# Kernel optimization log

Measured on AMD Instinct MI355X. Metric: run time of the kernel, lower is better.

The kernel has to match this reference:

```python
import jax, jax.numpy as jnp
import numpy as np

HID = 1024
H = 8        # num_attention_heads
KV = 2       # num_key_value_heads
HD = HID // H  # head_dim = 128
G = H // KV    # kv groups = 4
EPS = 1e-6


def setup_inputs() -> dict:
    key = jax.random.key(0)
    ks = jax.random.split(key, 12)
    B, S = 4, 2048
    s = 0.02
    inp = {
        "hidden_states": jax.random.normal(ks[0], (B, S, HID), jnp.float32),
        "rope": jax.random.normal(ks[1], (1, 1, S, 2 * HD), jnp.float32),
        # q_proj outputs 2*H*HD (query + elementwise gate)
        "Wq": jax.random.normal(ks[2], (HID, 2 * H * HD), jnp.float32) * s,
        "bq": jnp.zeros((2 * H * HD,), jnp.float32),
        "Wk": jax.random.normal(ks[3], (HID, KV * HD), jnp.float32) * s,
        "bk": jnp.zeros((KV * HD,), jnp.float32),
        "Wv": jax.random.normal(ks[4], (HID, KV * HD), jnp.float32) * s,
        "bv": jnp.zeros((KV * HD,), jnp.float32),
        "Wo": jax.random.normal(ks[5], (H * HD, HID), jnp.float32) * s,
        "bo": jnp.zeros((HID,), jnp.float32),
        "q_norm_w": jnp.ones((HD,), jnp.float32),
        "k_norm_w": jnp.ones((HD,), jnp.float32),
    }
    return inp


def _rmsnorm(x, w):
    var = jnp.mean(jnp.square(x), axis=-1, keepdims=True)
    return x * jax.lax.rsqrt(var + EPS) * w


def _rot(x):
    # interleaved rotation: [-x1, x0, -x3, x2, ...]
    x2 = x.reshape(x.shape[:-1] + (HD // 2, 2))
    r = jnp.stack([-x2[..., 1], x2[..., 0]], axis=-1)
    return r.reshape(x.shape)


def _apply_rope_cat(x, emb):
    # emb: [S, 2*HD] = cat(sin, cos); x: [B, h, S, HD]
    sin, cos = jnp.split(emb, 2, axis=-1)
    sin = sin[None, None]
    cos = cos[None, None]
    return x * cos + _rot(x) * sin


def reference(hidden_states, rope, Wq, bq, Wk, bk, Wv, bv, Wo, bo, q_norm_w, k_norm_w):
    B, S, _ = hidden_states.shape
    qg = hidden_states @ Wq + bq                     # [B,S,2*H*HD]
    qg = qg.reshape(B, S, KV, -1)                    # [B,S,KV, 2*G*HD]
    q, gate = jnp.split(qg, [HD * G], axis=-1)       # [B,S,KV,G*HD], [B,S,KV,G*HD]
    gate = gate.reshape(B, S, H, HD)                 # [B,S,H,HD]
    q = q.reshape(B, S, H, HD).transpose(0, 2, 1, 3) # [B,H,S,HD]
    k = (hidden_states @ Wk + bk).reshape(B, S, KV, HD).transpose(0, 2, 1, 3)
    v = (hidden_states @ Wv + bv).reshape(B, S, KV, HD).transpose(0, 2, 1, 3)

    q = _rmsnorm(q, q_norm_w)
    k = _rmsnorm(k, k_norm_w)

    emb = rope[0, 0, :S]                             # [S, 2*HD]
    q = _apply_rope_cat(q, emb)
    k = _apply_rope_cat(k, emb)

    # GQA: repeat kv heads to match query heads
    k = jnp.repeat(k, G, axis=1)                     # [B,H,S,HD]
    v = jnp.repeat(v, G, axis=1)

    scale = 1.0 / jnp.sqrt(jnp.asarray(HD, q.dtype))
    scores = jnp.einsum("bhqd,bhkd->bhqk", q, k) * scale
    attn = jax.nn.softmax(scores, axis=-1)
    out = jnp.einsum("bhqk,bhkd->bhqd", attn, v)     # [B,H,S,HD]

    out = out.transpose(0, 2, 1, 3)                  # [B,S,H,HD]
    out = out * jax.nn.sigmoid(gate)
    out = out.reshape(B, S, H * HD)
    return out @ Wo + bo
```

## Files before the change

### kernel.cpp

```cpp
#include <hip/hip_runtime.h>
#include <math.h>

#define SCALE_ 0.08838834764831845f
#define PSHIFT 8.0f

typedef __attribute__((ext_vector_type(8))) short short8;
typedef __attribute__((ext_vector_type(4))) float floatx4;
typedef __attribute__((ext_vector_type(4))) _Float16 half4;
typedef __attribute__((ext_vector_type(8))) _Float16 half8;

__device__ inline short f2bf(float x) {
    union { float f; unsigned u; } v; v.f = x;
    unsigned r = v.u + 0x7fff + ((v.u >> 16) & 1);
    return (short)(r >> 16);
}
__device__ inline float bf2f(short h) {
    union { float f; unsigned u; } v; v.u = ((unsigned)(unsigned short)h) << 16;
    return v.f;
}

__global__ __launch_bounds__(256) void prep_fused(
    const float* __restrict__ X, short* __restrict__ Xb,
    const float* __restrict__ bq, const float* __restrict__ bk2,
    const float* __restrict__ bv2, float* __restrict__ bcat,
    const float* __restrict__ Wq, const float* __restrict__ Wk,
    const float* __restrict__ Wv, const float* __restrict__ Wo,
    short* __restrict__ Wt, short* __restrict__ Wot)
{
    __shared__ float T[32][33];
    const int bid = blockIdx.x;
    const int t = threadIdx.x;
    if (bid < 8192) {
        const int gid = bid * 256 + t;
        if (gid < 2097152) {
            const float4 v = ((const float4*)X)[gid];
            short4 o;
            o.x = f2bf(v.x); o.y = f2bf(v.y); o.z = f2bf(v.z); o.w = f2bf(v.w);
            ((short4*)Xb)[gid] = o;
        }
        if (gid < 2560)
            bcat[gid] = (gid < 2048) ? bq[gid]
                      : (gid < 2304) ? bk2[gid - 2048] : bv2[gid - 2304];
        return;
    }
    const int t2 = bid - 8192;
    const int k0 = (t2 & 31) * 32;
    const int ny = t2 >> 5;
    const float* src; int ldn, ncol0, nrow0; short* dst;
    if (ny < 80) {
        const int n0 = ny * 32;
        if (n0 < 2048)      { src = Wq; ldn = 2048; ncol0 = n0; }
        else if (n0 < 2304) { src = Wk; ldn = 256;  ncol0 = n0 - 2048; }
        else                { src = Wv; ldn = 256;  ncol0 = n0 - 2304; }
        dst = Wt; nrow0 = n0;
    } else {
        const int n0 = (ny - 80) * 32;
        src = Wo; ldn = 1024; ncol0 = n0; dst = Wot; nrow0 = n0;
    }
    {
        const int r = t >> 3, c4 = (t & 7) * 4;
        const float4 v = *(const float4*)&src[(size_t)(k0 + r) * ldn + ncol0 + c4];
        T[r][c4 + 0] = v.x; T[r][c4 + 1] = v.y; T[r][c4 + 2] = v.z; T[r][c4 + 3] = v.w;
    }
    __syncthreads();
    {
        const int nr = t >> 3, kc4 = (t & 7) * 4;
        short4 o;
        o.x = f2bf(T[kc4 + 0][nr]);
        o.y = f2bf(T[kc4 + 1][nr]);
        o.z = f2bf(T[kc4 + 2][nr]);
        o.w = f2bf(T[kc4 + 3][nr]);
        *(short4*)&dst[(size_t)(nrow0 + nr) * 1024 + k0 + kc4] = o;
    }
}

__global__ __launch_bounds__(256) void qkv_mfma(
    const short* __restrict__ Ag, const short* __restrict__ Bg,
    const float* __restrict__ bcat,
    short* __restrict__ qb, short* __restrict__ kb,
    short* __restrict__ vb, short* __restrict__ gateb)
{
    __shared__ short As[128 * 64];
    __shared__ short Bs[128 * 64];
    const int tid = threadIdx.x;
    const int wave = tid >> 6, lane = tid & 63;
    const int quad = lane >> 4, l16 = lane & 15;
    const int wm = wave & 1, wn = wave >> 1;
    const int lin = blockIdx.x;
    const int xcd = lin & 7;
    const int idx = lin >> 3;
    const int rr_ = idx / 20;
    const int m0 = (xcd * 8 + rr_) * 128;
    const int n0 = (idx - rr_ * 20) * 128;

    floatx4 acc[4][4] = {};

    for (int k0 = 0; k0 < 1024; k0 += 64) {
        __syncthreads();
        #pragma unroll
        for (int c = 0; c < 4; ++c) {
            const int blk = (c * 4 + wave) * 64 + lane;
            const int row = blk >> 3, p = blk & 7;
            const int col = (p ^ (row & 7)) << 3;
            __builtin_amdgcn_global_load_lds(
                (const __attribute__((address_space(1))) unsigned int*)(Ag + (size_t)(m0 + row) * 1024 + k0 + col),
                (__attribute__((address_space(3))) unsigned int*)&As[(c * 4 + wave) * 512],
                16, 0, 0);
            __builtin_amdgcn_global_load_lds(
                (const __attribute__((address_space(1))) unsigned int*)(Bg + (size_t)(n0 + row) * 1024 + k0 + col),
                (__attribute__((address_space(3))) unsigned int*)&Bs[(c * 4 + wave) * 512],
                16, 0, 0);
        }
        __syncthreads();
        #pragma unroll
        for (int ks = 0; ks < 2; ++ks) {
            short8 af[4], bfr[4];
            #pragma unroll
            for (int mt = 0; mt < 4; ++mt) {
                const int row = wm * 64 + mt * 16 + l16;
                const int p = (ks * 4 + quad) ^ (row & 7);
                af[mt] = *(const short8*)&As[row * 64 + p * 8];
            }
            #pragma unroll
            for (int nt = 0; nt < 4; ++nt) {
                const int row = wn * 64 + nt * 16 + l16;
                const int p = (ks * 4 + quad) ^ (row & 7);
                bfr[nt] = *(const short8*)&Bs[row * 64 + p * 8];
            }
            #pragma unroll
            for (int mt = 0; mt < 4; ++mt)
                #pragma unroll
                for (int nt = 0; nt < 4; ++nt)
                    acc[mt][nt] = __builtin_amdgcn_mfma_f32_16x16x32_bf16(af[mt], bfr[nt], acc[mt][nt], 0, 0, 0);
        }
    }

    #pragma unroll
    for (int nt = 0; nt < 4; ++nt) {
        const int n = n0 + wn * 64 + nt * 16 + l16;
        const float bias = bcat[n];
        #pragma unroll
        for (int mt = 0; mt < 4; ++mt) {
            #pragma unroll
            for (int r = 0; r < 4; ++r) {
                const int m = m0 + wm * 64 + mt * 16 + quad * 4 + r;
                const int b = m >> 11, s = m & 2047;
                const short o = f2bf(acc[mt][nt][r] + bias);
                if (n < 2048) {
                    const int kv = n >> 10, rr = n & 1023;
                    if (rr < 512) {
                        const int h = kv * 4 + (rr >> 7), d = rr & 127;
                        qb[(((size_t)(b * 8 + h)) * 2048 + s) * 128 + d] = o;
                    } else {
                        const int r2 = rr - 512;
                        const int h = kv * 4 + (r2 >> 7), d = r2 & 127;
                        gateb[(size_t)m * 1024 + h * 128 + d] = o;
                    }
                } else if (n < 2304) {
                    const int c = n - 2048;
                    kb[(((size_t)(b * 2 + (c >> 7))) * 2048 + s) * 128 + (c & 127)] = o;
                } else {
                    const int c = n - 2304;
                    vb[(((size_t)(b * 2 + (c >> 7))) * 2048 + s) * 128 + (c & 127)] = o;
                }
            }
        }
    }
}

__global__ __launch_bounds__(256) void norm_vtrans(
    short* __restrict__ qb, short* __restrict__ kb,
    const float* __restrict__ rope,
    const float* __restrict__ qw, const float* __restrict__ kw,
    const short* __restrict__ vb, _Float16* __restrict__ vt)
{
    __shared__ float T[32][33];
    const int bid = blockIdx.x;
    const int t = threadIdx.x;
    if (bid < 20480) {
        const int row = bid * 4 + (t >> 6);
        short* base; const float* w; int s; float scl;
        if (row < 65536) { base = qb + (size_t)row * 128; s = row & 2047; w = qw; scl = SCALE_; }
        else { const int r2 = row - 65536; base = kb + (size_t)r2 * 128; s = r2 & 2047; w = kw; scl = 1.0f; }
        const int lane = t & 63;
        const short2 xv = *(const short2*)&base[lane * 2];
        const float x0 = bf2f(xv.x), x1 = bf2f(xv.y);
        float ssq = x0 * x0 + x1 * x1;
        #pragma unroll
        for (int off = 1; off < 64; off <<= 1) ssq += __shfl_xor(ssq, off);
        const float inv = rsqrtf(ssq * (1.0f / 128.0f) + 1e-6f);
        const float a = x0 * inv * w[lane * 2];
        const float b = x1 * inv * w[lane * 2 + 1];
        const float* er = rope + (size_t)s * 256;
        const float sin0 = er[lane * 2], sin1 = er[lane * 2 + 1];
        const float cos0 = er[128 + lane * 2], cos1 = er[128 + lane * 2 + 1];
        short2 o;
        o.x = f2bf((a * cos0 - b * sin0) * scl);
        o.y = f2bf((b * cos1 + a * sin1) * scl);
        *(short2*)&base[lane * 2] = o;
        return;
    }
    const int t2 = bid - 20480;
    const int s0 = (t2 & 63) * 32, d0 = ((t2 >> 6) & 3) * 32, bk = t2 >> 8;
    const short* src = vb + ((size_t)bk * 2048 + s0) * 128 + d0;
    {
        const int sr = t >> 3, c4 = (t & 7) * 4;
        const short4 xv = *(const short4*)&src[sr * 128 + c4];
        T[sr][c4 + 0] = bf2f(xv.x);
        T[sr][c4 + 1] = bf2f(xv.y);
        T[sr][c4 + 2] = bf2f(xv.z);
        T[sr][c4 + 3] = bf2f(xv.w);
    }
    __syncthreads();
    {
        const int dr = t >> 3, sc4 = (t & 7) * 4;
        const int cs = sc4 >> 2;
        const int nc = (cs < 4) ? (cs << 1) : (((cs - 4) << 1) | 1);
        half4 o;
        o[0] = (_Float16)T[sc4 + 0][dr];
        o[1] = (_Float16)T[sc4 + 1][dr];
        o[2] = (_Float16)T[sc4 + 2][dr];
        o[3] = (_Float16)T[sc4 + 3][dr];
        *(half4*)&vt[((size_t)bk * 128 + d0 + dr) * 2048 + s0 + nc * 4] = o;
    }
}

__global__ __launch_bounds__(256, 2) void attn_mfma(
    const short* __restrict__ qb, const short* __restrict__ kb,
    const _Float16* __restrict__ vt, const short* __restrict__ gateb,
    short* __restrict__ xo)
{
    __shared__ short    Ks[2][64 * 128];
    __shared__ _Float16 VTs[2][128 * 64];

    const int tid = threadIdx.x;
    const int wave = tid >> 6, lane = tid & 63;
    const int quad = lane >> 4, l16 = lane & 15;
    const int bh = blockIdx.y, b = bh >> 3, h = bh & 7, kv = h >> 2;
    const int q0 = blockIdx.x * 128;

    short8 qf[4][2];
    #pragma unroll
    for (int u = 0; u < 2; ++u) {
        const short* qbase = qb + (((size_t)(b * 8 + h)) * 2048 + q0 + wave * 32 + u * 16 + l16) * 128;
        #pragma unroll
        for (int ks = 0; ks < 4; ++ks)
            qf[ks][u] = *(const short8*)&qbase[ks * 32 + quad * 8];
    }

    const short*    kbase  = kb + (size_t)(b * 2 + kv) * 2048 * 128;
    const _Float16* vtbase = vt + (size_t)(b * 2 + kv) * 128 * 2048;

    int koff[4], voff[4];
    #pragma unroll
    for (int c = 0; c < 4; ++c) {
        const int sidx = (c * 4 + wave) * 64 + lane;
        { const int r = sidx >> 4, p = sidx & 15;
          koff[c] = r * 128 + ((p ^ (r & 7)) << 3); }
        { const int r = sidx >> 3, p = sidx & 7;
          voff[c] = r * 2048 + ((p ^ (r & 7)) << 3); }
    }

    floatx4 O[8][2] = {};
    float lsum[2] = {0.0f, 0.0f};

    #pragma unroll
    for (int c = 0; c < 4; ++c) {
        __builtin_amdgcn_global_load_lds(
            (const __attribute__((address_space(1))) unsigned int*)(kbase + koff[c]),
            (__attribute__((address_space(3))) unsigned int*)&Ks[0][(c * 4 + wave) * 512],
            16, 0, 0);
        __builtin_amdgcn_global_load_lds(
            (const __attribute__((address_space(1))) unsigned int*)(vtbase + voff[c]),
            (__attribute__((address_space(3))) unsigned int*)&VTs[0][(c * 4 + wave) * 512],
            16, 0, 0);
    }

    for (int kt = 0; kt < 32; ++kt) {
        const int cur = kt & 1;
        __syncthreads();

        if (kt + 1 < 32) {
            const short*    kg = kbase  + (size_t)(kt + 1) * 8192;
            const _Float16* vg = vtbase + (kt + 1) * 64;
            #pragma unroll
            for (int c = 0; c < 4; ++c) {
                __builtin_amdgcn_global_load_lds(
                    (const __attribute__((address_space(1))) unsigned int*)(kg + koff[c]),
                    (__attribute__((address_space(3))) unsigned int*)&Ks[cur ^ 1][(c * 4 + wave) * 512],
                    16, 0, 0);
                __builtin_amdgcn_global_load_lds(
                    (const __attribute__((address_space(1))) unsigned int*)(vg + voff[c]),
                    (__attribute__((address_space(3))) unsigned int*)&VTs[cur ^ 1][(c * 4 + wave) * 512],
                    16, 0, 0);
            }
        }

        #pragma unroll
        for (int t = 0; t < 2; ++t) {
            floatx4 ST[2][2];
            #pragma unroll
            for (int j = 0; j < 2; ++j) {
                ST[j][0] = (floatx4){0.f, 0.f, 0.f, 0.f};
                ST[j][1] = (floatx4){0.f, 0.f, 0.f, 0.f};
                const int krow = (2 * t + j) * 16 + l16;
                #pragma unroll
                for (int ks = 0; ks < 4; ++ks) {
                    const short8 af = *(const short8*)&Ks[cur][krow * 128 + (((ks * 4 + quad) ^ (l16 & 7)) << 3)];
                    ST[j][0] = __builtin_amdgcn_mfma_f32_16x16x32_bf16(af, qf[ks][0], ST[j][0], 0, 0, 0);
                    ST[j][1] = __builtin_amdgcn_mfma_f32_16x16x32_bf16(af, qf[ks][1], ST[j][1], 0, 0, 0);
                }
            }

            half8 pf[2];
            #pragma unroll
            for (int u = 0; u < 2; ++u) {
                #pragma unroll
                for (int r = 0; r < 4; ++r) {
                    const float plo = __expf(ST[0][u][r] - PSHIFT);
                    const float phi = __expf(ST[1][u][r] - PSHIFT);
                    lsum[u] += plo + phi;
                    pf[u][r]     = (_Float16)plo;
                    pf[u][4 + r] = (_Float16)phi;
                }
            }

            #pragma unroll
            for (int dt = 0; dt < 8; ++dt) {
                const half8 va = *(const half8*)&VTs[cur][(dt * 16 + l16) * 64 + (((4 * t + quad) ^ (l16 & 7)) << 3)];
                O[dt][0] = __builtin_amdgcn_mfma_f32_16x16x32_f16(va, pf[0], O[dt][0], 0, 0, 0);
                O[dt][1] = __builtin_amdgcn_mfma_f32_16x16x32_f16(va, pf[1], O[dt][1], 0, 0, 0);
            }
        }
    }

    #pragma unroll
    for (int u = 0; u < 2; ++u) {
        float ps = lsum[u];
        ps += __shfl_xor(ps, 16);
        ps += __shfl_xor(ps, 32);
        const float invl = 1.0f / ps;
        const int s = q0 + wave * 32 + u * 16 + l16;
        const size_t base = ((size_t)b * 2048 + s) * 1024 + h * 128;
        #pragma unroll
        for (int dt = 0; dt < 8; ++dt) {
            const int d0 = dt * 16 + quad * 4;
            const short4 g4 = *(const short4*)&gateb[base + d0];
            short4 o4;
            o4.x = f2bf(O[dt][u][0] * invl * (1.0f / (1.0f + __expf(-bf2f(g4.x)))));
            o4.y = f2bf(O[dt][u][1] * invl * (1.0f / (1.0f + __expf(-bf2f(g4.y)))));
            o4.z = f2bf(O[dt][u][2] * invl * (1.0f / (1.0f + __expf(-bf2f(g4.z)))));
            o4.w = f2bf(O[dt][u][3] * invl * (1.0f / (1.0f + __expf(-bf2f(g4.w)))));
            *(short4*)&xo[base + d0] = o4;
        }
    }
}

__global__ __launch_bounds__(256) void out_mfma(
    const short* __restrict__ Ag, const short* __restrict__ Bg,
    const float* __restrict__ bo, float* __restrict__ Y)
{
    __shared__ short As[128 * 64];
    __shared__ short Bs[128 * 64];
    const int tid = threadIdx.x;
    const int wave = tid >> 6, lane = tid & 63;
    const int quad = lane >> 4, l16 = lane & 15;
    const int wm = wave & 1, wn = wave >> 1;
    const int lin = blockIdx.x;
    const int xcd = lin & 7;
    const int idx = lin >> 3;
    const int m0 = (xcd * 8 + (idx >> 3)) * 128;
    const int n0 = (idx & 7) * 128;

    floatx4 acc[4][4] = {};

    for (int k0 = 0; k0 < 1024; k0 += 64) {
        __syncthreads();
        #pragma unroll
        for (int c = 0; c < 4; ++c) {
            const int blk = (c * 4 + wave) * 64 + lane;
            const int row = blk >> 3, p = blk & 7;
            const int col = (p ^ (row & 7)) << 3;
            __builtin_amdgcn_global_load_lds(
                (const __attribute__((address_space(1))) unsigned int*)(Ag + (size_t)(m0 + row) * 1024 + k0 + col),
                (__attribute__((address_space(3))) unsigned int*)&As[(c * 4 + wave) * 512],
                16, 0, 0);
            __builtin_amdgcn_global_load_lds(
                (const __attribute__((address_space(1))) unsigned int*)(Bg + (size_t)(n0 + row) * 1024 + k0 + col),
                (__attribute__((address_space(3))) unsigned int*)&Bs[(c * 4 + wave) * 512],
                16, 0, 0);
        }
        __syncthreads();
        #pragma unroll
        for (int ks = 0; ks < 2; ++ks) {
            short8 af[4], bfr[4];
            #pragma unroll
            for (int mt = 0; mt < 4; ++mt) {
                const int row = wm * 64 + mt * 16 + l16;
                const int p = (ks * 4 + quad) ^ (row & 7);
                af[mt] = *(const short8*)&As[row * 64 + p * 8];
            }
            #pragma unroll
            for (int nt = 0; nt < 4; ++nt) {
                const int row = wn * 64 + nt * 16 + l16;
                const int p = (ks * 4 + quad) ^ (row & 7);
                bfr[nt] = *(const short8*)&Bs[row * 64 + p * 8];
            }
            #pragma unroll
            for (int mt = 0; mt < 4; ++mt)
                #pragma unroll
                for (int nt = 0; nt < 4; ++nt)
                    acc[mt][nt] = __builtin_amdgcn_mfma_f32_16x16x32_bf16(af[mt], bfr[nt], acc[mt][nt], 0, 0, 0);
        }
    }

    #pragma unroll
    for (int nt = 0; nt < 4; ++nt) {
        const int n = n0 + wn * 64 + nt * 16 + l16;
        const float bias = bo[n];
        #pragma unroll
        for (int mt = 0; mt < 4; ++mt) {
            #pragma unroll
            for (int r = 0; r < 4; ++r) {
                const int m = m0 + wm * 64 + mt * 16 + quad * 4 + r;
                Y[(size_t)m * 1024 + n] = acc[mt][nt][r] + bias;
            }
        }
    }
}

extern "C" void kernel_launch(void* const* d_in, const int* in_sizes, int n_in,
                              void* d_out, int out_size, void* d_ws, size_t ws_size,
                              hipStream_t stream) {
    (void)in_sizes; (void)n_in; (void)out_size; (void)ws_size;
    const float* hs   = (const float*)d_in[0];
    const float* rope = (const float*)d_in[1];
    const float* Wq   = (const float*)d_in[2];
    const float* bq   = (const float*)d_in[3];
    const float* Wk   = (const float*)d_in[4];
    const float* bk   = (const float*)d_in[5];
    const float* Wv   = (const float*)d_in[6];
    const float* bv   = (const float*)d_in[7];
    const float* Wo   = (const float*)d_in[8];
    const float* bo   = (const float*)d_in[9];
    const float* qw   = (const float*)d_in[10];
    const float* kw   = (const float*)d_in[11];
    float* out = (float*)d_out;

    short* qb    = (short*)d_ws;
    short* kbuf  = qb    + (size_t)8388608;
    short* vb    = kbuf  + (size_t)2097152;
    _Float16* vt = (_Float16*)(vb + (size_t)2097152);
    short* gateb = (short*)(vt + (size_t)2097152);
    short* xb    = gateb + (size_t)8388608;
    short* wt    = xb    + (size_t)8388608;
    short* wot   = wt    + (size_t)2621440;
    float* bcat  = (float*)(wot + (size_t)1048576);

    prep_fused<<<dim3(11776), 256, 0, stream>>>(hs, xb, bq, bk, bv, bcat,
                                                Wq, Wk, Wv, Wo, wt, wot);
    qkv_mfma<<<dim3(1280), 256, 0, stream>>>(xb, wt, bcat, qb, kbuf, vb, gateb);
    norm_vtrans<<<dim3(22528), 256, 0, stream>>>(qb, kbuf, rope, qw, kw, vb, vt);
    attn_mfma<<<dim3(16, 32), 256, 0, stream>>>(qb, kbuf, vt, gateb, xb);
    out_mfma<<<dim3(512), 256, 0, stream>>>(xb, wot, bo, out);
}
```

Baseline: 296.5 us.

## Fuse RMSNorm, RoPE and V transpose into QKV GEMM epilogue

The separate norm_vtrans kernel is removed. The QKV GEMM epilogue now applies RMSNorm through a cross-wave reduction in shared memory, applies RoPE using a lane shuffle to fetch each interleaved partner value, and writes V transposed in fp16 through a shared scratch tile. This saves one launch and a full read-modify-write pass over q/k/v in global memory. In exchange the GEMM uses more shared memory (roughly 17KB extra), which may lower occupancy, and it adds extra barriers in the epilogue.

```diff
diff --git a/kernel.cpp b/kernel.cpp
--- a/kernel.cpp
+++ b/kernel.cpp
@@ -77,11 +77,15 @@
 __global__ __launch_bounds__(256) void qkv_mfma(
     const short* __restrict__ Ag, const short* __restrict__ Bg,
     const float* __restrict__ bcat,
+    const float* __restrict__ rope,
+    const float* __restrict__ qw, const float* __restrict__ kw,
     short* __restrict__ qb, short* __restrict__ kb,
-    short* __restrict__ vb, short* __restrict__ gateb)
+    _Float16* __restrict__ vt, short* __restrict__ gateb)
 {
     __shared__ short As[128 * 64];
     __shared__ short Bs[128 * 64];
+    __shared__ _Float16 vscr[128 * 68];
+    __shared__ float sred[256];
     const int tid = threadIdx.x;
     const int wave = tid >> 6, lane = tid & 63;
     const int quad = lane >> 4, l16 = lane & 15;
@@ -135,93 +139,126 @@
         }
     }
 
+    const int dl0 = wn * 64 + l16;
+    float bias4[4];
     #pragma unroll
-    for (int nt = 0; nt < 4; ++nt) {
-        const int n = n0 + wn * 64 + nt * 16 + l16;
-        const float bias = bcat[n];
-        #pragma unroll
-        for (int mt = 0; mt < 4; ++mt) {
+    for (int nt = 0; nt < 4; ++nt) bias4[nt] = bcat[n0 + dl0 + nt * 16];
+    const int nlow = n0 & 1023;
+
+    if (n0 >= 2304) {
+        const int kvv = (n0 - 2304) >> 7;
+        const int bV = m0 >> 11, s0g = m0 & 2047;
+        const size_t vtb = ((size_t)(bV * 2 + kvv)) * 128 * 2048;
+        __syncthreads();
+        #pragma unroll
+        for (int half = 0; half < 2; ++half) {
+            if (wn == half) {
+                #pragma unroll
+                for (int mt = 0; mt < 4; ++mt)
+                    #pragma unroll
+                    for (int r = 0; r < 4; ++r) {
+                        const int sl = wm * 64 + mt * 16 + quad * 4 + r;
+                        #pragma unroll
+                        for (int nt = 0; nt < 4; ++nt)
+                            vscr[sl * 68 + nt * 16 + l16] =
+                                (_Float16)(acc[mt][nt][r] + bias4[nt]);
+                    }
+            }
+            __syncthreads();
+            {
+                const int dl = tid & 63, sch = tid >> 6;
+                #pragma unroll
+                for (int g = 0; g < 8; ++g) {
+                    half4 o;
+                    #pragma unroll
+                    for (int e = 0; e < 4; ++e)
+                        o[e] = vscr[(sch * 32 + g * 4 + e) * 68 + dl];
+                    const int ncs = (g < 4) ? (g << 1) : (((g - 4) << 1) | 1);
+                    *(half4*)&vt[vtb + (size_t)(half * 64 + dl) * 2048 + s0g + sch * 32 + ncs * 4] = o;
+                }
+            }
+            __syncthreads();
+        }
+    } else if (n0 < 2048 && nlow >= 512) {
+        const int h = ((n0 >> 10) << 2) + ((nlow - 512) >> 7);
+        #pragma unroll
+        for (int nt = 0; nt < 4; ++nt) {
+            const int d = dl0 + nt * 16;
+            #pragma unroll
+            for (int mt = 0; mt < 4; ++mt)
+                #pragma unroll
+                for (int r = 0; r < 4; ++r) {
+                    const int m = m0 + wm * 64 + mt * 16 + quad * 4 + r;
+                    gateb[(size_t)m * 1024 + h * 128 + d] = f2bf(acc[mt][nt][r] + bias4[nt]);
+                }
+        }
+    } else {
+        const int isQ = (n0 < 2048);
+        const int hq  = isQ ? (((n0 >> 10) << 2) + (nlow >> 7)) : 0;
+        const int kvk = isQ ? 0 : ((n0 - 2048) >> 7);
+        const float* wv = isQ ? qw : kw;
+        const float scl = isQ ? SCALE_ : 1.0f;
+        short* dst = isQ ? qb : kb;
+
+        __syncthreads();
+        float part[4][4];
+        #pragma unroll
+        for (int mt = 0; mt < 4; ++mt)
+            #pragma unroll
+            for (int r = 0; r < 4; ++r) {
+                float p = 0.f;
+                #pragma unroll
+                for (int nt = 0; nt < 4; ++nt) {
+                    const float x = acc[mt][nt][r] + bias4[nt];
+                    p += x * x;
+                }
+                #pragma unroll
+                for (int off = 1; off < 16; off <<= 1)
+                    p += __shfl_xor(p, off);
+                part[mt][r] = p;
+            }
+        if (wn == 1 && l16 == 0) {
+            #pragma unroll
+            for (int mt = 0; mt < 4; ++mt)
+                #pragma unroll
+                for (int r = 0; r < 4; ++r)
+                    sred[wm * 64 + mt * 16 + quad * 4 + r] = part[mt][r];
+        }
+        __syncthreads();
+        if (wn == 0 && l16 == 0) {
+            #pragma unroll
+            for (int mt = 0; mt < 4; ++mt)
+                #pragma unroll
+                for (int r = 0; r < 4; ++r) {
+                    const int ml = wm * 64 + mt * 16 + quad * 4 + r;
+                    const float tot = part[mt][r] + sred[ml];
+                    sred[128 + ml] = rsqrtf(tot * (1.0f / 128.0f) + 1e-6f);
+                }
+        }
+        __syncthreads();
+        float w4[4];
+        #pragma unroll
+        for (int nt = 0; nt < 4; ++nt) w4[nt] = wv[dl0 + nt * 16];
+        #pragma unroll
+        for (int mt = 0; mt < 4; ++mt)
             #pragma unroll
             for (int r = 0; r < 4; ++r) {
                 const int m = m0 + wm * 64 + mt * 16 + quad * 4 + r;
-                const int b = m >> 11, s = m & 2047;
-                const short o = f2bf(acc[mt][nt][r] + bias);
-                if (n < 2048) {
-                    const int kv = n >> 10, rr = n & 1023;
-                    if (rr < 512) {
-                        const int h = kv * 4 + (rr >> 7), d = rr & 127;
-                        qb[(((size_t)(b * 8 + h)) * 2048 + s) * 128 + d] = o;
-                    } else {
-                        const int r2 = rr - 512;
-                        const int h = kv * 4 + (r2 >> 7), d = r2 & 127;
-                        gateb[(size_t)m * 1024 + h * 128 + d] = o;
-                    }
-                } else if (n < 2304) {
-                    const int c = n - 2048;
-                    kb[(((size_t)(b * 2 + (c >> 7))) * 2048 + s) * 128 + (c & 127)] = o;
-                } else {
-                    const int c = n - 2304;
-                    vb[(((size_t)(b * 2 + (c >> 7))) * 2048 + s) * 128 + (c & 127)] = o;
-                }
-            }
-        }
-    }
-}
-
-__global__ __launch_bounds__(256) void norm_vtrans(
-    short* __restrict__ qb, short* __restrict__ kb,
-    const float* __restrict__ rope,
-    const float* __restrict__ qw, const float* __restrict__ kw,
-    const short* __restrict__ vb, _Float16* __restrict__ vt)
-{
-    __shared__ float T[32][33];
-    const int bid = blockIdx.x;
-    const int t = threadIdx.x;
-    if (bid < 20480) {
-        const int row = bid * 4 + (t >> 6);
-        short* base; const float* w; int s; float scl;
-        if (row < 65536) { base = qb + (size_t)row * 128; s = row & 2047; w = qw; scl = SCALE_; }
-        else { const int r2 = row - 65536; base = kb + (size_t)r2 * 128; s = r2 & 2047; w = kw; scl = 1.0f; }
-        const int lane = t & 63;
-        const short2 xv = *(const short2*)&base[lane * 2];
-        const float x0 = bf2f(xv.x), x1 = bf2f(xv.y);
-        float ssq = x0 * x0 + x1 * x1;
-        #pragma unroll
-        for (int off = 1; off < 64; off <<= 1) ssq += __shfl_xor(ssq, off);
-        const float inv = rsqrtf(ssq * (1.0f / 128.0f) + 1e-6f);
-        const float a = x0 * inv * w[lane * 2];
-        const float b = x1 * inv * w[lane * 2 + 1];
-        const float* er = rope + (size_t)s * 256;
-        const float sin0 = er[lane * 2], sin1 = er[lane * 2 + 1];
-        const float cos0 = er[128 + lane * 2], cos1 = er[128 + lane * 2 + 1];
-        short2 o;
-        o.x = f2bf((a * cos0 - b * sin0) * scl);
-        o.y = f2bf((b * cos1 + a * sin1) * scl);
-        *(short2*)&base[lane * 2] = o;
-        return;
-    }
-    const int t2 = bid - 20480;
-    const int s0 = (t2 & 63) * 32, d0 = ((t2 >> 6) & 3) * 32, bk = t2 >> 8;
-    const short* src = vb + ((size_t)bk * 2048 + s0) * 128 + d0;
-    {
-        const int sr = t >> 3, c4 = (t & 7) * 4;
-        const short4 xv = *(const short4*)&src[sr * 128 + c4];
-        T[sr][c4 + 0] = bf2f(xv.x);
-        T[sr][c4 + 1] = bf2f(xv.y);
-        T[sr][c4 + 2] = bf2f(xv.z);
-        T[sr][c4 + 3] = bf2f(xv.w);
-    }
-    __syncthreads();
-    {
-        const int dr = t >> 3, sc4 = (t & 7) * 4;
-        const int cs = sc4 >> 2;
-        const int nc = (cs < 4) ? (cs << 1) : (((cs - 4) << 1) | 1);
-        half4 o;
-        o[0] = (_Float16)T[sc4 + 0][dr];
-        o[1] = (_Float16)T[sc4 + 1][dr];
-        o[2] = (_Float16)T[sc4 + 2][dr];
-        o[3] = (_Float16)T[sc4 + 3][dr];
-        *(half4*)&vt[((size_t)bk * 128 + d0 + dr) * 2048 + s0 + nc * 4] = o;
+                const int bb = m >> 11, s = m & 2047;
+                const float inv = sred[128 + wm * 64 + mt * 16 + quad * 4 + r];
+                const float* er = rope + (size_t)s * 256;
+                const size_t rb = ((size_t)(isQ ? (bb * 8 + hq) : (bb * 2 + kvk)) * 2048 + s) * 128;
+                #pragma unroll
+                for (int nt = 0; nt < 4; ++nt) {
+                    const int d = dl0 + nt * 16;
+                    const float xn = (acc[mt][nt][r] + bias4[nt]) * inv * w4[nt];
+                    const float pn = __shfl_xor(xn, 1);
+                    const float sn = er[d], cn = er[128 + d];
+                    const float out = (l16 & 1) ? fmaf(xn, cn, pn * sn)
+                                                : fmaf(xn, cn, -pn * sn);
+                    dst[rb + d] = f2bf(out * scl);
+                }
+            }
     }
 }
 
@@ -459,8 +496,8 @@
 
     prep_fused<<<dim3(11776), 256, 0, stream>>>(hs, xb, bq, bk, bv, bcat,
                                                 Wq, Wk, Wv, Wo, wt, wot);
-    qkv_mfma<<<dim3(1280), 256, 0, stream>>>(xb, wt, bcat, qb, kbuf, vb, gateb);
-    norm_vtrans<<<dim3(22528), 256, 0, stream>>>(qb, kbuf, rope, qw, kw, vb, vt);
+    qkv_mfma<<<dim3(1280), 256, 0, stream>>>(xb, wt, bcat, rope, qw, kw,
+                                             qb, kbuf, vt, gateb);
     attn_mfma<<<dim3(16, 32), 256, 0, stream>>>(qb, kbuf, vt, gateb, xb);
     out_mfma<<<dim3(512), 256, 0, stream>>>(xb, wot, bo, out);
 }
```

Result: faster. 283.8 us (median of 3 runs) (-4.3%).
